# Kernel optimization log

Measured on AMD Instinct MI355X. Metric: run time of the kernel, lower is better.

The kernel has to match this reference:

```python
import jax, jax.numpy as jnp
import numpy as np

ROT_ERR_W = 15.0   # weight[0]
TRANS_ERR_W = 100.0  # weight[1]
CONV_ROT = 0.0
CONV_TRANS = 0.0
EPS = 1e-7
SMALL = 1e-4


def _skew(w):
    # w: [..., 3] -> [..., 3, 3]
    z = jnp.zeros_like(w[..., 0])
    r0 = jnp.stack([z, -w[..., 2], w[..., 1]], axis=-1)
    r1 = jnp.stack([w[..., 2], z, -w[..., 0]], axis=-1)
    r2 = jnp.stack([-w[..., 1], w[..., 0], z], axis=-1)
    return jnp.stack([r0, r1, r2], axis=-2)


def _log_se3(R, t):
    # SE(3) log map. R: [...,3,3], t: [...,3] -> (theta, omega[...,3], v[...,3])
    tr = R[..., 0, 0] + R[..., 1, 1] + R[..., 2, 2]
    cos_t = jnp.clip((tr - 1.0) * 0.5, -1.0 + EPS, 1.0 - EPS)
    theta = jnp.arccos(cos_t)
    sin_t = jnp.sin(theta)
    # vee(R - R^T)/2
    w_vee = 0.5 * jnp.stack([
        R[..., 2, 1] - R[..., 1, 2],
        R[..., 0, 2] - R[..., 2, 0],
        R[..., 1, 0] - R[..., 0, 1],
    ], axis=-1)
    small = theta < SMALL
    safe_sin = jnp.where(small, 1.0, sin_t)
    scale = jnp.where(small, 1.0 + theta * theta / 6.0, theta / safe_sin)
    omega = scale[..., None] * w_vee
    # V^{-1} t -> translational twist
    wx = _skew(omega)
    wx2 = jnp.matmul(wx, wx)
    theta2 = jnp.where(small, 1.0, theta * theta)
    A = jnp.where(
        small,
        jnp.full_like(theta, 1.0 / 12.0),
        (1.0 - (theta * sin_t) / (2.0 * (1.0 - cos_t))) / theta2,
    )
    Vinv = jnp.eye(3, dtype=R.dtype) - 0.5 * wx + A[..., None, None] * wx2
    v = jnp.einsum('...ij,...j->...i', Vinv, t)
    return theta, omega, v


def setup_inputs() -> dict:
    key = jax.random.key(0)
    k1, k2, k3, k4 = jax.random.split(key, 4)
    B, H = 2048, 2048  # n_particles x horizon
    return {
        'ee_pos_batch': jax.random.normal(k1, (B, H, 3), jnp.float32),
        'ee_rot_batch': jax.random.normal(k2, (B, H, 3, 3), jnp.float32),
        'ee_goal_pos': jax.random.normal(k3, (3,), jnp.float32),
        'ee_goal_rot': jax.random.normal(k4, (3, 3), jnp.float32),
        'vec_weight': jnp.ones((6,), jnp.float32),
    }


def reference(ee_pos_batch, ee_rot_batch, ee_goal_pos, ee_goal_rot, vec_weight):
    # goal_to_ee = inverse(ee_to_world) * goal_to_world
    Rt = jnp.swapaxes(ee_rot_batch, -1, -2)                 # R_ee^T, [B,H,3,3]
    R_ge = jnp.matmul(Rt, ee_goal_rot)                       # [B,H,3,3]
    t_ge = jnp.einsum('bhij,bhj->bhi', Rt, ee_goal_pos - ee_pos_batch)
    _, omega, v = _log_se3(R_ge, t_ge)
    # squared_l2 NormCost with unit weight
    position_err = jnp.sum(jnp.square(vec_weight[3:6] * v), axis=-1)
    rotation_err = jnp.sum(jnp.square(vec_weight[0:3] * omega), axis=-1)
    rotation_err = jnp.where(rotation_err < CONV_ROT, 0.0, rotation_err)
    position_err = jnp.where(position_err < CONV_TRANS, 0.0, position_err)
    cost = ROT_ERR_W * rotation_err + TRANS_ERR_W * position_err
    return cost, rotation_err, position_err, v, omega
```

## Files before the change

kernel.cpp:

```cpp
#include <hip/hip_runtime.h>


#define BLOCK 256

typedef float f32x4 __attribute__((ext_vector_type(4)));

__device__ __forceinline__ void pose_one(
    const float* R, float p0, float p1, float p2,
    const float* G, float g0, float g1, float g2, const float* w,
    float& cost, float& re, float& pe,
    float& v0, float& v1, float& v2,
    float& o0, float& o1, float& o2)
{
    const float d0 = g0 - p0, d1 = g1 - p1, d2 = g2 - p2;
    const float tq0 = R[0] * d0 + R[3] * d1 + R[6] * d2;
    const float tq1 = R[1] * d0 + R[4] * d1 + R[7] * d2;
    const float tq2 = R[2] * d0 + R[5] * d1 + R[8] * d2;

    float M[9];
    #pragma unroll
    for (int i = 0; i < 3; ++i)
        #pragma unroll
        for (int j = 0; j < 3; ++j)
            M[i * 3 + j] = R[0 + i] * G[0 + j] + R[3 + i] * G[3 + j] + R[6 + i] * G[6 + j];

    const float tr = M[0] + M[4] + M[8];
    float cos_t = (tr - 1.0f) * 0.5f;
    cos_t = fminf(fmaxf(cos_t, -1.0f + 1e-7f), 1.0f - 1e-7f);
    const float theta = acosf(cos_t);
    const float sin_t = sqrtf(fmaf(-cos_t, cos_t, 1.0f));

    const float wv0 = 0.5f * (M[7] - M[5]);
    const float wv1 = 0.5f * (M[2] - M[6]);
    const float wv2 = 0.5f * (M[3] - M[1]);

    const bool small = theta < 1e-4f;
    const float th2 = theta * theta;
    const float scale = small ? (1.0f + th2 * (1.0f / 6.0f)) : (theta / sin_t);
    o0 = scale * wv0; o1 = scale * wv1; o2 = scale * wv2;

    const float A = small ? (1.0f / 12.0f)
                          : (1.0f - 0.5f * scale * (1.0f + cos_t)) / th2;

    const float cx0 = o1 * tq2 - o2 * tq1;
    const float cx1 = o2 * tq0 - o0 * tq2;
    const float cx2 = o0 * tq1 - o1 * tq0;
    const float odt = o0 * tq0 + o1 * tq1 + o2 * tq2;
    const float on2 = o0 * o0 + o1 * o1 + o2 * o2;
    v0 = tq0 - 0.5f * cx0 + A * (o0 * odt - on2 * tq0);
    v1 = tq1 - 0.5f * cx1 + A * (o1 * odt - on2 * tq1);
    v2 = tq2 - 0.5f * cx2 + A * (o2 * odt - on2 * tq2);

    const float we0 = w[0] * o0, we1 = w[1] * o1, we2 = w[2] * o2;
    const float wp0 = w[3] * v0, wp1 = w[4] * v1, wp2 = w[5] * v2;
    re = we0 * we0 + we1 * we1 + we2 * we2;
    pe = wp0 * wp0 + wp1 * wp1 + wp2 * wp2;
    re = (re < 0.0f) ? 0.0f : re;
    pe = (pe < 0.0f) ? 0.0f : pe;
    cost = 15.0f * re + 100.0f * pe;
}

__global__ __launch_bounds__(BLOCK) void pose_cost_kernel(
    const float* __restrict__ pos,
    const float* __restrict__ rot,
    const float* __restrict__ gpos,
    const float* __restrict__ grot,
    const float* __restrict__ wvec,
    float* __restrict__ out,
    int N)
{
    const size_t tid = (size_t)blockIdx.x * BLOCK + threadIdx.x;
    const size_t i0 = tid * 4;
    if (i0 >= (size_t)N) return;

    float G[9], w[6];
    #pragma unroll
    for (int k = 0; k < 9; ++k) G[k] = grot[k];
    const float g0 = gpos[0], g1 = gpos[1], g2 = gpos[2];
    #pragma unroll
    for (int k = 0; k < 6; ++k) w[k] = wvec[k];

    const size_t Ns = (size_t)N;

    if (((N & 3) == 0)) {
        const f32x4* rs = reinterpret_cast<const f32x4*>(rot + i0 * 9);
        const f32x4* ps = reinterpret_cast<const f32x4*>(pos + i0 * 3);
        f32x4 r[9], p[3];
        #pragma unroll
        for (int k = 0; k < 9; ++k) r[k] = rs[k];
        #pragma unroll
        for (int k = 0; k < 3; ++k) p[k] = ps[k];

        #define RF(q) (r[(q) >> 2][(q) & 3])
        #define PF(q) (p[(q) >> 2][(q) & 3])

        f32x4 vcost, vre, vpe;
        f32x4 vv[3], vo[3];
        #define VV(q) (vv[(q) >> 2][(q) & 3])
        #define VO(q) (vo[(q) >> 2][(q) & 3])

        #pragma unroll
        for (int j = 0; j < 4; ++j) {
            float R[9];
            #pragma unroll
            for (int k = 0; k < 9; ++k) R[k] = RF(9 * j + k);
            const float p0 = PF(3 * j + 0);
            const float p1 = PF(3 * j + 1);
            const float p2 = PF(3 * j + 2);

            float c, re, pe, v0, v1, v2, o0, o1, o2;
            pose_one(R, p0, p1, p2, G, g0, g1, g2, w,
                     c, re, pe, v0, v1, v2, o0, o1, o2);
            vcost[j] = c; vre[j] = re; vpe[j] = pe;
            VV(3 * j + 0) = v0; VV(3 * j + 1) = v1; VV(3 * j + 2) = v2;
            VO(3 * j + 0) = o0; VO(3 * j + 1) = o1; VO(3 * j + 2) = o2;
        }
        #undef RF
        #undef PF
        #undef VV
        #undef VO

        *reinterpret_cast<f32x4*>(out + i0) = vcost;
        *reinterpret_cast<f32x4*>(out + Ns + i0) = vre;
        *reinterpret_cast<f32x4*>(out + 2 * Ns + i0) = vpe;
        f32x4* vd = reinterpret_cast<f32x4*>(out + 3 * Ns + i0 * 3);
        f32x4* od = reinterpret_cast<f32x4*>(out + 6 * Ns + i0 * 3);
        #pragma unroll
        for (int k = 0; k < 3; ++k) vd[k] = vv[k];
        #pragma unroll
        for (int k = 0; k < 3; ++k) od[k] = vo[k];
    } else {
        const size_t iend = (i0 + 4 < Ns) ? (i0 + 4) : Ns;
        for (size_t i = i0; i < iend; ++i) {
            float R[9];
            #pragma unroll
            for (int k = 0; k < 9; ++k) R[k] = rot[i * 9 + k];
            const float p0 = pos[i * 3 + 0];
            const float p1 = pos[i * 3 + 1];
            const float p2 = pos[i * 3 + 2];

            float c, re, pe, v0, v1, v2, o0, o1, o2;
            pose_one(R, p0, p1, p2, G, g0, g1, g2, w,
                     c, re, pe, v0, v1, v2, o0, o1, o2);

            out[i] = c;
            out[Ns + i] = re;
            out[2 * Ns + i] = pe;
            out[3 * Ns + i * 3 + 0] = v0;
            out[3 * Ns + i * 3 + 1] = v1;
            out[3 * Ns + i * 3 + 2] = v2;
            out[6 * Ns + i * 3 + 0] = o0;
            out[6 * Ns + i * 3 + 1] = o1;
            out[6 * Ns + i * 3 + 2] = o2;
        }
    }
}

extern "C" void kernel_launch(void* const* d_in, const int* in_sizes, int n_in,
                              void* d_out, int out_size, void* d_ws, size_t ws_size,
                              hipStream_t stream) {
    const float* pos  = (const float*)d_in[0];
    const float* rot  = (const float*)d_in[1];
    const float* gpos = (const float*)d_in[2];
    const float* grot = (const float*)d_in[3];
    const float* wv   = (const float*)d_in[4];
    float* out = (float*)d_out;

    const int N = in_sizes[0] / 3;
    const int nthreads = (N + 3) / 4;
    const int blocks = (nthreads + BLOCK - 1) / BLOCK;
    hipLaunchKernelGGL(pose_cost_kernel, dim3(blocks), dim3(BLOCK), 0, stream,
                       pos, rot, gpos, grot, wv, out, N);
}
```

Measured before the change: 296.2 us.

## Use persistent grid-stride loop with double-buffered register prefetch

The launch now uses a fixed grid of 512 blocks instead of one thread per four poses, and each thread walks chunks with a grid stride. Loads for the next chunk are issued into a second register buffer while the current chunk is computed, so memory latency can overlap with the transcendental math. This doubles the input registers held per thread, which may lower occupancy, and the smaller grid may leave less parallelism to hide latency on a large GPU.

```diff
diff --git a/kernel.cpp b/kernel.cpp
--- a/kernel.cpp
+++ b/kernel.cpp
@@ -2,6 +2,7 @@
 
 
 #define BLOCK 256
+#define GRID_BLOCKS 512
 
 typedef float f32x4 __attribute__((ext_vector_type(4)));
 
@@ -60,6 +61,62 @@
     cost = 15.0f * re + 100.0f * pe;
 }
 
+__device__ __forceinline__ void load_chunk(
+    f32x4 (&r)[9], f32x4 (&p)[3],
+    const float* __restrict__ rot, const float* __restrict__ pos, size_t c)
+{
+    const f32x4* rs = reinterpret_cast<const f32x4*>(rot + c * 36);
+    const f32x4* ps = reinterpret_cast<const f32x4*>(pos + c * 12);
+    #pragma unroll
+    for (int k = 0; k < 9; ++k) r[k] = rs[k];
+    #pragma unroll
+    for (int k = 0; k < 3; ++k) p[k] = ps[k];
+}
+
+__device__ __forceinline__ void process_chunk(
+    const f32x4 (&r)[9], const f32x4 (&p)[3], size_t c, size_t Ns,
+    const float (&G)[9], float g0, float g1, float g2, const float (&w)[6],
+    float* __restrict__ out)
+{
+    f32x4 vcost, vre, vpe, vv[3], vo[3];
+
+    #define RF(q) (r[(q) >> 2][(q) & 3])
+    #define PF(q) (p[(q) >> 2][(q) & 3])
+    #define VV(q) (vv[(q) >> 2][(q) & 3])
+    #define VO(q) (vo[(q) >> 2][(q) & 3])
+
+    #pragma unroll
+    for (int j = 0; j < 4; ++j) {
+        float R[9];
+        #pragma unroll
+        for (int k = 0; k < 9; ++k) R[k] = RF(9 * j + k);
+        const float p0 = PF(3 * j + 0);
+        const float p1 = PF(3 * j + 1);
+        const float p2 = PF(3 * j + 2);
+
+        float cst, re, pe, v0, v1, v2, o0, o1, o2;
+        pose_one(R, p0, p1, p2, G, g0, g1, g2, w,
+                 cst, re, pe, v0, v1, v2, o0, o1, o2);
+        vcost[j] = cst; vre[j] = re; vpe[j] = pe;
+        VV(3 * j + 0) = v0; VV(3 * j + 1) = v1; VV(3 * j + 2) = v2;
+        VO(3 * j + 0) = o0; VO(3 * j + 1) = o1; VO(3 * j + 2) = o2;
+    }
+    #undef RF
+    #undef PF
+    #undef VV
+    #undef VO
+
+    *reinterpret_cast<f32x4*>(out + 4 * c) = vcost;
+    *reinterpret_cast<f32x4*>(out + Ns + 4 * c) = vre;
+    *reinterpret_cast<f32x4*>(out + 2 * Ns + 4 * c) = vpe;
+    f32x4* vd = reinterpret_cast<f32x4*>(out + 3 * Ns + 12 * c);
+    f32x4* od = reinterpret_cast<f32x4*>(out + 6 * Ns + 12 * c);
+    #pragma unroll
+    for (int k = 0; k < 3; ++k) vd[k] = vv[k];
+    #pragma unroll
+    for (int k = 0; k < 3; ++k) od[k] = vo[k];
+}
+
 __global__ __launch_bounds__(BLOCK) void pose_cost_kernel(
     const float* __restrict__ pos,
     const float* __restrict__ rot,
@@ -69,9 +126,9 @@
     float* __restrict__ out,
     int N)
 {
+    const size_t nthr = (size_t)gridDim.x * BLOCK;
     const size_t tid = (size_t)blockIdx.x * BLOCK + threadIdx.x;
-    const size_t i0 = tid * 4;
-    if (i0 >= (size_t)N) return;
+    const size_t Ns = (size_t)N;
 
     float G[9], w[6];
     #pragma unroll
@@ -80,58 +137,29 @@
     #pragma unroll
     for (int k = 0; k < 6; ++k) w[k] = wvec[k];
 
-    const size_t Ns = (size_t)N;
-
-    if (((N & 3) == 0)) {
-        const f32x4* rs = reinterpret_cast<const f32x4*>(rot + i0 * 9);
-        const f32x4* ps = reinterpret_cast<const f32x4*>(pos + i0 * 3);
-        f32x4 r[9], p[3];
-        #pragma unroll
-        for (int k = 0; k < 9; ++k) r[k] = rs[k];
-        #pragma unroll
-        for (int k = 0; k < 3; ++k) p[k] = ps[k];
-
-        #define RF(q) (r[(q) >> 2][(q) & 3])
-        #define PF(q) (p[(q) >> 2][(q) & 3])
-
-        f32x4 vcost, vre, vpe;
-        f32x4 vv[3], vo[3];
-        #define VV(q) (vv[(q) >> 2][(q) & 3])
-        #define VO(q) (vo[(q) >> 2][(q) & 3])
-
-        #pragma unroll
-        for (int j = 0; j < 4; ++j) {
-            float R[9];
-            #pragma unroll
-            for (int k = 0; k < 9; ++k) R[k] = RF(9 * j + k);
-            const float p0 = PF(3 * j + 0);
-            const float p1 = PF(3 * j + 1);
-            const float p2 = PF(3 * j + 2);
-
-            float c, re, pe, v0, v1, v2, o0, o1, o2;
-            pose_one(R, p0, p1, p2, G, g0, g1, g2, w,
-                     c, re, pe, v0, v1, v2, o0, o1, o2);
-            vcost[j] = c; vre[j] = re; vpe[j] = pe;
-            VV(3 * j + 0) = v0; VV(3 * j + 1) = v1; VV(3 * j + 2) = v2;
-            VO(3 * j + 0) = o0; VO(3 * j + 1) = o1; VO(3 * j + 2) = o2;
+    if ((N & 3) == 0) {
+        const size_t CH = Ns / 4;
+        f32x4 rA[9], pA[3], rB[9], pB[3];
+
+        size_t cA = tid;
+        if (cA < CH) {
+            load_chunk(rA, pA, rot, pos, cA);
+            for (;;) {
+                const size_t cB = cA + nthr;
+                const bool hasB = cB < CH;
+                if (hasB) load_chunk(rB, pB, rot, pos, cB);
+                process_chunk(rA, pA, cA, Ns, G, g0, g1, g2, w, out);
+                if (!hasB) break;
+                const size_t cN = cB + nthr;
+                const bool hasA = cN < CH;
+                if (hasA) load_chunk(rA, pA, rot, pos, cN);
+                process_chunk(rB, pB, cB, Ns, G, g0, g1, g2, w, out);
+                if (!hasA) break;
+                cA = cN;
+            }
         }
-        #undef RF
-        #undef PF
-        #undef VV
-        #undef VO
-
-        *reinterpret_cast<f32x4*>(out + i0) = vcost;
-        *reinterpret_cast<f32x4*>(out + Ns + i0) = vre;
-        *reinterpret_cast<f32x4*>(out + 2 * Ns + i0) = vpe;
-        f32x4* vd = reinterpret_cast<f32x4*>(out + 3 * Ns + i0 * 3);
-        f32x4* od = reinterpret_cast<f32x4*>(out + 6 * Ns + i0 * 3);
-        #pragma unroll
-        for (int k = 0; k < 3; ++k) vd[k] = vv[k];
-        #pragma unroll
-        for (int k = 0; k < 3; ++k) od[k] = vo[k];
     } else {
-        const size_t iend = (i0 + 4 < Ns) ? (i0 + 4) : Ns;
-        for (size_t i = i0; i < iend; ++i) {
+        for (size_t i = tid; i < Ns; i += nthr) {
             float R[9];
             #pragma unroll
             for (int k = 0; k < 9; ++k) R[k] = rot[i * 9 + k];
@@ -139,11 +167,11 @@
             const float p1 = pos[i * 3 + 1];
             const float p2 = pos[i * 3 + 2];
 
-            float c, re, pe, v0, v1, v2, o0, o1, o2;
+            float cst, re, pe, v0, v1, v2, o0, o1, o2;
             pose_one(R, p0, p1, p2, G, g0, g1, g2, w,
-                     c, re, pe, v0, v1, v2, o0, o1, o2);
-
-            out[i] = c;
+                     cst, re, pe, v0, v1, v2, o0, o1, o2);
+
+            out[i] = cst;
             out[Ns + i] = re;
             out[2 * Ns + i] = pe;
             out[3 * Ns + i * 3 + 0] = v0;
@@ -167,8 +195,9 @@
     float* out = (float*)d_out;
 
     const int N = in_sizes[0] / 3;
-    const int nthreads = (N + 3) / 4;
-    const int blocks = (nthreads + BLOCK - 1) / BLOCK;
+    int blocks = GRID_BLOCKS;
+    const int maxNeeded = (int)(((size_t)N + 4 * BLOCK - 1) / (4 * BLOCK));
+    if (blocks > maxNeeded) blocks = maxNeeded > 0 ? maxNeeded : 1;
     hipLaunchKernelGGL(pose_cost_kernel, dim3(blocks), dim3(BLOCK), 0, stream,
                        pos, rot, gpos, grot, wv, out, N);
 }
```

New measurement: 299.5 us. About the same (+1.1%).

## Stage inputs via async global-to-LDS loads with persistent double-buffered tiles

Applied to the files above, without the earlier changes.

Replaces the one-shot 4-poses-per-thread kernel with a persistent grid (at most 2048 blocks) that loops over 256-pose tiles. Each tile's rotation and position data is copied into LDS with global_load_lds, double-buffered so the next tiles load while the current one computes. Threads then read their poses from LDS, giving coalesced global reads. The cost is scalar, non-vectorised output stores, extra barriers per tile, and LDS bank conflicts from the stride-9 reads.

```diff
diff --git a/kernel.cpp b/kernel.cpp
--- a/kernel.cpp
+++ b/kernel.cpp
@@ -1,9 +1,19 @@
 #include <hip/hip_runtime.h>
+#include <stdint.h>
 
 
 #define BLOCK 256
+#define TILE  256
+#define MAXB  2048
 
 typedef float f32x4 __attribute__((ext_vector_type(4)));
+
+__device__ __forceinline__ void gload_lds16(const float* g, float* l) {
+    __builtin_amdgcn_global_load_lds(
+        (const __attribute__((address_space(1))) void*)g,
+        (__attribute__((address_space(3))) void*)l,
+        16 , 0 , 0 );
+}
 
 __device__ __forceinline__ void pose_one(
     const float* R, float p0, float p1, float p2,
@@ -69,9 +79,12 @@
     float* __restrict__ out,
     int N)
 {
-    const size_t tid = (size_t)blockIdx.x * BLOCK + threadIdx.x;
-    const size_t i0 = tid * 4;
-    if (i0 >= (size_t)N) return;
+    __shared__ float buf[2][3 * TILE * 4];
+
+    const int t = threadIdx.x;
+    const int wave = t >> 6;
+    const int lane = t & 63;
+    const size_t Ns = (size_t)N;
 
     float G[9], w[6];
     #pragma unroll
@@ -80,58 +93,73 @@
     #pragma unroll
     for (int k = 0; k < 6; ++k) w[k] = wvec[k];
 
-    const size_t Ns = (size_t)N;
-
-    if (((N & 3) == 0)) {
-        const f32x4* rs = reinterpret_cast<const f32x4*>(rot + i0 * 9);
-        const f32x4* ps = reinterpret_cast<const f32x4*>(pos + i0 * 3);
-        f32x4 r[9], p[3];
-        #pragma unroll
-        for (int k = 0; k < 9; ++k) r[k] = rs[k];
-        #pragma unroll
-        for (int k = 0; k < 3; ++k) p[k] = ps[k];
-
-        #define RF(q) (r[(q) >> 2][(q) & 3])
-        #define PF(q) (p[(q) >> 2][(q) & 3])
-
-        f32x4 vcost, vre, vpe;
-        f32x4 vv[3], vo[3];
-        #define VV(q) (vv[(q) >> 2][(q) & 3])
-        #define VO(q) (vo[(q) >> 2][(q) & 3])
-
-        #pragma unroll
-        for (int j = 0; j < 4; ++j) {
+    if ((N % TILE) == 0 && N > 0) {
+        const size_t T  = Ns / TILE;
+        const size_t Gd = gridDim.x;
+        const size_t b  = blockIdx.x;
+        const size_t cnt = (T - b + Gd - 1) / Gd;
+
+        auto stage = [&](float* dst, size_t tile) {
+            #pragma unroll
+            for (int i2 = 0; i2 < 3; ++i2) {
+                const int c = wave + 4 * i2;
+                const float* g = (c < 9)
+                    ? (rot + tile * (size_t)(9 * TILE) + (size_t)c * 256 + (size_t)lane * 4)
+                    : (pos + tile * (size_t)(3 * TILE) + (size_t)(c - 9) * 256 + (size_t)lane * 4);
+                gload_lds16(g, dst + c * 256 + lane * 4);
+            }
+        };
+        auto tileAt = [&](size_t j) {
+            const size_t jj = (j < cnt) ? j : (cnt - 1);
+            return b + jj * Gd;
+        };
+
+        stage(buf[0], tileAt(0));
+        __builtin_amdgcn_sched_barrier(0);
+        stage(buf[1], tileAt(1));
+        __builtin_amdgcn_sched_barrier(0);
+
+        for (size_t i = 0; i < cnt; ++i) {
+            asm volatile("s_waitcnt vmcnt(3)" ::: "memory");
+            __builtin_amdgcn_sched_barrier(0);
+            __builtin_amdgcn_s_barrier();
+
+            const float* bb = buf[i & 1];
+            const size_t tile = b + i * Gd;
+            const size_t idx = tile * TILE + (size_t)t;
+
             float R[9];
             #pragma unroll
-            for (int k = 0; k < 9; ++k) R[k] = RF(9 * j + k);
-            const float p0 = PF(3 * j + 0);
-            const float p1 = PF(3 * j + 1);
-            const float p2 = PF(3 * j + 2);
-
-            float c, re, pe, v0, v1, v2, o0, o1, o2;
+            for (int k = 0; k < 9; ++k) R[k] = bb[t * 9 + k];
+            const float p0 = bb[2304 + t * 3 + 0];
+            const float p1 = bb[2304 + t * 3 + 1];
+            const float p2 = bb[2304 + t * 3 + 2];
+
+            float cst, re, pe, v0, v1, v2, o0, o1, o2;
             pose_one(R, p0, p1, p2, G, g0, g1, g2, w,
-                     c, re, pe, v0, v1, v2, o0, o1, o2);
-            vcost[j] = c; vre[j] = re; vpe[j] = pe;
-            VV(3 * j + 0) = v0; VV(3 * j + 1) = v1; VV(3 * j + 2) = v2;
-            VO(3 * j + 0) = o0; VO(3 * j + 1) = o1; VO(3 * j + 2) = o2;
+                     cst, re, pe, v0, v1, v2, o0, o1, o2);
+
+            out[idx] = cst;
+            out[Ns + idx] = re;
+            out[2 * Ns + idx] = pe;
+            out[3 * Ns + idx * 3 + 0] = v0;
+            out[3 * Ns + idx * 3 + 1] = v1;
+            out[3 * Ns + idx * 3 + 2] = v2;
+            out[6 * Ns + idx * 3 + 0] = o0;
+            out[6 * Ns + idx * 3 + 1] = o1;
+            out[6 * Ns + idx * 3 + 2] = o2;
+
+            asm volatile("s_waitcnt lgkmcnt(0)" ::: "memory");
+            __builtin_amdgcn_sched_barrier(0);
+            __builtin_amdgcn_s_barrier();
+
+            stage(buf[i & 1], tileAt(i + 2));
+            __builtin_amdgcn_sched_barrier(0);
         }
-        #undef RF
-        #undef PF
-        #undef VV
-        #undef VO
-
-        *reinterpret_cast<f32x4*>(out + i0) = vcost;
-        *reinterpret_cast<f32x4*>(out + Ns + i0) = vre;
-        *reinterpret_cast<f32x4*>(out + 2 * Ns + i0) = vpe;
-        f32x4* vd = reinterpret_cast<f32x4*>(out + 3 * Ns + i0 * 3);
-        f32x4* od = reinterpret_cast<f32x4*>(out + 6 * Ns + i0 * 3);
-        #pragma unroll
-        for (int k = 0; k < 3; ++k) vd[k] = vv[k];
-        #pragma unroll
-        for (int k = 0; k < 3; ++k) od[k] = vo[k];
     } else {
-        const size_t iend = (i0 + 4 < Ns) ? (i0 + 4) : Ns;
-        for (size_t i = i0; i < iend; ++i) {
+        const size_t nthr = (size_t)gridDim.x * BLOCK;
+        const size_t tid = (size_t)blockIdx.x * BLOCK + t;
+        for (size_t i = tid; i < Ns; i += nthr) {
             float R[9];
             #pragma unroll
             for (int k = 0; k < 9; ++k) R[k] = rot[i * 9 + k];
@@ -139,11 +167,11 @@
             const float p1 = pos[i * 3 + 1];
             const float p2 = pos[i * 3 + 2];
 
-            float c, re, pe, v0, v1, v2, o0, o1, o2;
+            float cst, re, pe, v0, v1, v2, o0, o1, o2;
             pose_one(R, p0, p1, p2, G, g0, g1, g2, w,
-                     c, re, pe, v0, v1, v2, o0, o1, o2);
-
-            out[i] = c;
+                     cst, re, pe, v0, v1, v2, o0, o1, o2);
+
+            out[i] = cst;
             out[Ns + i] = re;
             out[2 * Ns + i] = pe;
             out[3 * Ns + i * 3 + 0] = v0;
@@ -167,8 +195,14 @@
     float* out = (float*)d_out;
 
     const int N = in_sizes[0] / 3;
-    const int nthreads = (N + 3) / 4;
-    const int blocks = (nthreads + BLOCK - 1) / BLOCK;
+    int blocks;
+    if (N > 0 && (N % TILE) == 0) {
+        const long long T = (long long)N / TILE;
+        blocks = (int)((T < MAXB) ? T : MAXB);
+    } else {
+        const long long need = ((long long)N + BLOCK - 1) / BLOCK;
+        blocks = (int)((need < MAXB) ? (need > 0 ? need : 1) : MAXB);
+    }
     hipLaunchKernelGGL(pose_cost_kernel, dim3(blocks), dim3(BLOCK), 0, stream,
                        pos, rot, gpos, grot, wv, out, N);
 }
```

New measurement: 300.6 us. About the same (+1.5%).
